# Optimization experiments

Measured on AMD Instinct MI355X. Metric: run time of the kernel, lower is better.

The kernel has to match this reference:

```python
import jax, jax.numpy as jnp
import numpy as np

L, E, S, H, D, V = 6, 384, 256, 6, 64, 65
FF = 4 * E


def _ln(x, g, b, ddof, eps=1e-5):
    mean = jnp.mean(x, axis=-1, keepdims=True)
    var = jnp.var(x, axis=-1, keepdims=True, ddof=ddof)
    return g * (x - mean) / jnp.sqrt(var + eps) + b


def setup_inputs() -> dict:
    key = jax.random.key(0)
    ks = jax.random.split(key, 16)
    std = 0.02
    inp = {
        'x': jax.random.randint(ks[0], (64, S), 0, V),
        'tok_emb': jax.random.normal(ks[1], (V, E)) * std,
        'pos_emb': jax.random.normal(ks[2], (S, E)) * std,
        'Wq': jax.random.normal(ks[3], (L, E, H * D)) * std,
        'Wk': jax.random.normal(ks[4], (L, E, H * D)) * std,
        'Wv': jax.random.normal(ks[5], (L, E, H * D)) * std,
        'Wproj': jax.random.normal(ks[6], (L, H * D, E)) * std,
        'bproj': jnp.zeros((L, E)),
        'W1': jax.random.normal(ks[7], (L, E, FF)) * std,
        'b1': jnp.zeros((L, FF)),
        'W2': jax.random.normal(ks[8], (L, FF, E)) * std,
        'b2': jnp.zeros((L, E)),
        'ln1_g': jnp.ones((L, E)), 'ln1_b': jnp.zeros((L, E)),
        'ln2_g': jnp.ones((L, E)), 'ln2_b': jnp.zeros((L, E)),
        'lnf_g': jnp.ones((E,)), 'lnf_b': jnp.zeros((E,)),
        'Wlm': jax.random.normal(ks[9], (E, V)) * std,
        'blm': jnp.zeros((V,)),
    }
    return inp


def _forward(x, tok_emb, pos_emb, Wq, Wk, Wv, Wproj, bproj, W1, b1, W2, b2,
             ln1_g, ln1_b, ln2_g, ln2_b, lnf_g, lnf_b, Wlm, blm):
    B, T = x.shape
    h = tok_emb[x] + pos_emb[:T]  # [B,T,E]
    causal = jnp.tril(jnp.ones((T, T), dtype=bool))
    neg_inf = jnp.finfo(h.dtype).min
    for l in range(L):
        hn = _ln(h, ln1_g[l], ln1_b[l], ddof=1)  # custom LayerNorm uses unbiased var
        q = (hn @ Wq[l]).reshape(B, T, H, D)
        k = (hn @ Wk[l]).reshape(B, T, H, D)
        v = (hn @ Wv[l]).reshape(B, T, H, D)
        wei = jnp.einsum('bqhd,bkhd->bhqk', q, k) * (D ** -0.5)
        wei = jnp.where(causal, wei, neg_inf)
        wei = jax.nn.softmax(wei, axis=-1)
        att = jnp.einsum('bhqk,bkhd->bqhd', wei, v).reshape(B, T, H * D)
        h = h + att @ Wproj[l] + bproj[l]
        hn = _ln(h, ln2_g[l], ln2_b[l], ddof=1)
        h = h + jax.nn.relu(hn @ W1[l] + b1[l]) @ W2[l] + b2[l]
    h = _ln(h, lnf_g, lnf_b, ddof=0)  # nn.LayerNorm uses biased var
    return h @ Wlm + blm  # logits [B,T,V]


def reference(x, tok_emb, pos_emb, Wq, Wk, Wv, Wproj, bproj, W1, b1, W2, b2,
              ln1_g, ln1_b, ln2_g, ln2_b, lnf_g, lnf_b, Wlm, blm):
    return _forward(x, tok_emb, pos_emb, Wq, Wk, Wv, Wproj, bproj, W1, b1, W2, b2,
                    ln1_g, ln1_b, ln2_g, ln2_b, lnf_g, lnf_b, Wlm, blm)
```

## Files before the change

### kernel.cpp

```cpp
#include <hip/hip_runtime.h>

#define L_  6
#define E_  384
#define T_  256
#define H_  6
#define D_  64
#define V_  65
#define FF_ 1536
#define B_  64
#define BT_ (B_*T_)
#define HD_ 384

typedef __attribute__((ext_vector_type(8))) short short8;
typedef __attribute__((ext_vector_type(4))) float f32x4;
typedef unsigned short us;
typedef unsigned int u32;

__device__ __forceinline__ us f2bf(float f) {
  u32 u = __float_as_uint(f);
  u32 r = (u + 0x7fffu + ((u >> 16) & 1u)) >> 16;
  return (us)r;
}
__device__ __forceinline__ float bf2f(us v) {
  return __uint_as_float(((u32)v) << 16);
}

__device__ __forceinline__ int xcd_swz(int b, int nwg) {
  const int q = nwg >> 3;
  return (b & 7) * q + (b >> 3);
}

__global__ void embed_kernel(const int* __restrict__ x, const float* __restrict__ tok,
                             const float* __restrict__ pos, us* __restrict__ h) {
  const int total8 = BT_ * E_ / 8;
  for (int i = blockIdx.x * blockDim.x + threadIdx.x; i < total8;
       i += gridDim.x * blockDim.x) {
    const int flat = i << 3;
    const int row  = flat / E_;
    const int e    = flat - row * E_;
    const int id   = x[row];
    const float4 a0 = *reinterpret_cast<const float4*>(tok + id * E_ + e);
    const float4 a1 = *reinterpret_cast<const float4*>(tok + id * E_ + e + 4);
    const float4 p0 = *reinterpret_cast<const float4*>(pos + (row & (T_ - 1)) * E_ + e);
    const float4 p1 = *reinterpret_cast<const float4*>(pos + (row & (T_ - 1)) * E_ + e + 4);
    short8 o;
    o[0] = (short)f2bf(a0.x + p0.x); o[1] = (short)f2bf(a0.y + p0.y);
    o[2] = (short)f2bf(a0.z + p0.z); o[3] = (short)f2bf(a0.w + p0.w);
    o[4] = (short)f2bf(a1.x + p1.x); o[5] = (short)f2bf(a1.y + p1.y);
    o[6] = (short)f2bf(a1.z + p1.z); o[7] = (short)f2bf(a1.w + p1.w);
    *reinterpret_cast<short8*>(h + flat) = o;
  }
}

template<int DDOF>
__global__ void stats_kernel(const us* __restrict__ h, float2* __restrict__ st) {
  const int wave = threadIdx.x >> 6;
  const int lane = threadIdx.x & 63;
  const int row  = (blockIdx.x << 2) + wave;
  float sum = 0.f, sq = 0.f;
  if (lane < 48) {
    const short8 v = *reinterpret_cast<const short8*>(h + (size_t)row * E_ + lane * 8);
#pragma unroll
    for (int j = 0; j < 8; ++j) {
      const float f = bf2f((us)v[j]);
      sum += f; sq += f * f;
    }
  }
#pragma unroll
  for (int off = 32; off > 0; off >>= 1) {
    sum += __shfl_xor(sum, off);
    sq  += __shfl_xor(sq, off);
  }
  if (lane == 0) {
    const float mean = sum * (1.f / E_);
    const float var  = (sq - E_ * mean * mean) * (1.f / (E_ - DDOF));
    float2 o; o.x = mean; o.y = rsqrtf(var + 1e-5f);
    st[row] = o;
  }
}

__global__ void transpose_w(const float* __restrict__ src, us* __restrict__ dst,
                            int K, int N, int Ndst, long srcLS, long dstLS,
                            const float* __restrict__ g) {
  __shared__ float t[32][33];
  const int n0 = blockIdx.x << 5, k0 = blockIdx.y << 5;
  const int tx = threadIdx.x & 31, ty = threadIdx.x >> 5;
  const float* s = src + (size_t)blockIdx.z * srcLS;
  us* d = dst + (size_t)blockIdx.z * dstLS;
#pragma unroll
  for (int j = 0; j < 32; j += 8) {
    const int n = n0 + tx;
    t[ty + j][tx] = (n < N) ? s[(size_t)(k0 + ty + j) * N + n] : 0.f;
  }
  __syncthreads();
  const float gk = g ? g[blockIdx.z * 384 + k0 + tx] : 1.f;
#pragma unroll
  for (int j = 0; j < 32; j += 8) {
    const int n = n0 + ty + j;
    if (n < Ndst) d[(size_t)n * K + k0 + tx] = f2bf(t[tx][ty + j] * gk);
  }
}

__global__ void transpose_qkv(const float* __restrict__ Wq, const float* __restrict__ Wk,
                              const float* __restrict__ Wv, us* __restrict__ dst,
                              const float* __restrict__ g) {
  __shared__ float t[32][33];
  const int sel = blockIdx.z / 6, l = blockIdx.z % 6;
  const float* s = (sel == 0 ? Wq : sel == 1 ? Wk : Wv) + (size_t)l * 147456;
  us* d = dst + (size_t)l * 442368 + sel * 147456;
  const int n0 = blockIdx.x << 5, k0 = blockIdx.y << 5;
  const int tx = threadIdx.x & 31, ty = threadIdx.x >> 5;
#pragma unroll
  for (int j = 0; j < 32; j += 8)
    t[ty + j][tx] = s[(size_t)(k0 + ty + j) * 384 + n0 + tx];
  __syncthreads();
  const float gk = g[l * 384 + k0 + tx];
#pragma unroll
  for (int j = 0; j < 32; j += 8)
    d[(size_t)(n0 + ty + j) * 384 + k0 + tx] = f2bf(t[tx][ty + j] * gk);
}

__global__ void c12_kernel(const float* __restrict__ W, const float* __restrict__ g,
                           const float* __restrict__ b, float2* __restrict__ out,
                           int N, long srcLS, int outLS) {
  __shared__ float p1[4][64], p2[4][64];
  const int t = threadIdx.x;
  const int c = t & 63, kq = t >> 6;
  const int n = (blockIdx.x << 6) + c;
  const float* Wz = W + (size_t)blockIdx.y * srcLS;
  const float* gz = g + blockIdx.y * 384;
  const float* bz = b + blockIdx.y * 384;
  float s1 = 0.f, s2 = 0.f;
  if (n < N) {
    for (int k = kq * 96; k < kq * 96 + 96; ++k) {
      const float w = Wz[(size_t)k * N + n];
      s1 = fmaf(gz[k], w, s1);
      s2 = fmaf(bz[k], w, s2);
    }
  }
  p1[kq][c] = s1; p2[kq][c] = s2;
  __syncthreads();
  if (t < 64) {
    const int nn = (blockIdx.x << 6) + t;
    if (nn < N) {
      float2 o;
      o.x = p1[0][t] + p1[1][t] + p1[2][t] + p1[3][t];
      o.y = p2[0][t] + p2[1][t] + p2[2][t] + p2[3][t];
      out[(size_t)blockIdx.y * outLS + nn] = o;
    }
  }
}

__global__ void c12_qkv(const float* __restrict__ Wq, const float* __restrict__ Wk,
                        const float* __restrict__ Wv, const float* __restrict__ g,
                        const float* __restrict__ b, float2* __restrict__ out) {
  __shared__ float p1[4][64], p2[4][64];
  const int sel = blockIdx.y / 6, l = blockIdx.y % 6;
  const float* Wz = (sel == 0 ? Wq : sel == 1 ? Wk : Wv) + (size_t)l * 147456;
  const float* gz = g + l * 384;
  const float* bz = b + l * 384;
  const int t = threadIdx.x;
  const int c = t & 63, kq = t >> 6;
  const int n = (blockIdx.x << 6) + c;
  float s1 = 0.f, s2 = 0.f;
  for (int k = kq * 96; k < kq * 96 + 96; ++k) {
    const float w = Wz[(size_t)k * 384 + n];
    s1 = fmaf(gz[k], w, s1);
    s2 = fmaf(bz[k], w, s2);
  }
  p1[kq][c] = s1; p2[kq][c] = s2;
  __syncthreads();
  if (t < 64) {
    const int nn = (blockIdx.x << 6) + t;
    float2 o;
    o.x = p1[0][t] + p1[1][t] + p1[2][t] + p1[3][t];
    o.y = p2[0][t] + p2[1][t] + p2[2][t] + p2[3][t];
    out[(size_t)l * 1152 + sel * 384 + nn] = o;
  }
}

template<int ROWS, int CHPR, int NTH>
__device__ __forceinline__ void stageG(const us* g, int rowUs, us* lds, int tid) {
#pragma unroll
  for (int j = 0; j < ROWS * CHPR / NTH; ++j) {
    const int fl  = j * NTH + tid;
    const int row = fl / CHPR;
    const int c   = fl % CHPR;
    const int gc  = (CHPR == 8) ? (c ^ (row & 7)) : (c ^ ((row >> 1) & 3));
    const us* src = g + (size_t)row * rowUs + gc * 8;
    __builtin_amdgcn_global_load_lds(
        (const __attribute__((address_space(1))) u32*)src,
        (__attribute__((address_space(3))) u32*)(lds + ((fl >> 6) << 9)),
        16, 0, 0);
  }
}

#define GEMM_LOOP(K_, NT_)                                                        \
  const int NT = (NT_);                                                           \
  _Pragma("unroll")                                                               \
  for (int p = 0; p < BUFS - 1; ++p) {                                            \
    stageG<BM, 4, 256>(Abase + p * 32, (K_), As[p], tid);                         \
    stageG<BN, 4, 256>(Bbase + p * 32, (K_), Bs[p], tid);                         \
  }                                                                               \
  int cb = 0;                                                                     \
  for (int t = 0; t < NT; ++t) {                                                  \
    if constexpr (BUFS == 4) {                                                    \
      if (t < NT - 2)       asm volatile("s_waitcnt vmcnt(%0)" :: "n"(2 * LPS) : "memory"); \
      else if (t == NT - 2) asm volatile("s_waitcnt vmcnt(%0)" :: "n"(LPS) : "memory");     \
      else                  asm volatile("s_waitcnt vmcnt(0)" ::: "memory");      \
    } else {                                                                      \
      if (t < NT - 1)       asm volatile("s_waitcnt vmcnt(%0)" :: "n"(LPS) : "memory");     \
      else                  asm volatile("s_waitcnt vmcnt(0)" ::: "memory");      \
    }                                                                             \
    __builtin_amdgcn_s_barrier();                                                 \
    __builtin_amdgcn_sched_barrier(0);                                            \
    if (t + BUFS - 1 < NT) {                                                      \
      int ib = cb + (BUFS - 1); if (ib >= BUFS) ib -= BUFS;                       \
      stageG<BM, 4, 256>(Abase + (t + BUFS - 1) * 32, (K_), As[ib], tid);         \
      stageG<BN, 4, 256>(Bbase + (t + BUFS - 1) * 32, (K_), Bs[ib], tid);         \
    }                                                                             \
    short8 af[FM], bfr[FN];                                                       \
    _Pragma("unroll")                                                             \
    for (int mt = 0; mt < FM; ++mt) {                                             \
      const int row = wm + mt * 16 + fm;                                          \
      af[mt] = *(const short8*)(As[cb] + row * 32 + ((fg ^ ((row >> 1) & 3)) << 3)); \
    }                                                                             \
    _Pragma("unroll")                                                             \
    for (int nt = 0; nt < FN; ++nt) {                                             \
      const int row = wn + nt * 16 + fm;                                          \
      bfr[nt] = *(const short8*)(Bs[cb] + row * 32 + ((fg ^ ((row >> 1) & 3)) << 3)); \
    }                                                                             \
    _Pragma("unroll")                                                             \
    for (int mt = 0; mt < FM; ++mt)                                               \
      _Pragma("unroll")                                                           \
      for (int nt = 0; nt < FN; ++nt)                                             \
        acc[mt][nt] = __builtin_amdgcn_mfma_f32_16x16x32_bf16(af[mt], bfr[nt], acc[mt][nt], 0, 0, 0); \
    cb = (cb + 1 == BUFS) ? 0 : cb + 1;                                           \
  }

template<int FM, int FN, int BUFS>
__global__ __launch_bounds__(256)
void gemm_mfma(const us* __restrict__ A, const us* __restrict__ Bt,
               const float* __restrict__ bias, const us* Res,
               us* __restrict__ O, int N, int K, int gx) {
  constexpr int BM = FM * 32, BN = FN * 32;
  constexpr int LPS = (BM + BN) * 4 / 256;
  __shared__ us As[BUFS][BM * 32];
  __shared__ us Bs[BUFS][BN * 32];
  const int tid = threadIdx.x;
  const int lid = xcd_swz(blockIdx.x, gridDim.x);
  const int bnI = lid % gx, bmI = lid / gx;
  const int bm = bmI * BM, bn = bnI * BN;
  const int wv = tid >> 6, ln = tid & 63;
  const int fm = ln & 15, fg = ln >> 4;
  const int wm = (wv >> 1) * (FM * 16), wn = (wv & 1) * (FN * 16);
  const us* Abase = A + (size_t)bm * K;
  const us* Bbase = Bt + (size_t)bn * K;

  f32x4 acc[FM][FN];
  const f32x4 zz = {0.f, 0.f, 0.f, 0.f};
#pragma unroll
  for (int i = 0; i < FM; ++i)
#pragma unroll
    for (int j = 0; j < FN; ++j) acc[i][j] = zz;

  GEMM_LOOP(K, K >> 5)

#pragma unroll
  for (int mt = 0; mt < FM; ++mt) {
#pragma unroll
    for (int nt = 0; nt < FN; ++nt) {
      const int col  = bn + wn + nt * 16 + fm;
      const int row0 = bm + wm + mt * 16 + fg * 4;
      const float bc = bias[col];
#pragma unroll
      for (int r = 0; r < 4; ++r) {
        const size_t idx = (size_t)(row0 + r) * N + col;
        O[idx] = f2bf(acc[mt][nt][r] + bc + bf2f(Res[idx]));
      }
    }
  }
}

template<int FM, int FN, int EPI, int BUFS>
__global__ __launch_bounds__(256)
void gemm_fold(const us* __restrict__ A, const us* __restrict__ Bt,
               const float2* __restrict__ st, const float2* __restrict__ c12,
               const float* __restrict__ bias, void* O0, void* O1,
               int N, int gx) {
  constexpr int K = 384;
  constexpr int BM = FM * 32, BN = FN * 32;
  constexpr int LPS = (BM + BN) * 4 / 256;
  __shared__ us As[BUFS][BM * 32];
  __shared__ us Bs[BUFS][BN * 32];
  const int tid = threadIdx.x;
  const int lid = xcd_swz(blockIdx.x, gridDim.x);
  const int bnI = lid % gx, bmI = lid / gx;
  const int bm = bmI * BM, bn = bnI * BN;
  const int wv = tid >> 6, ln = tid & 63;
  const int fm = ln & 15, fg = ln >> 4;
  const int wm = (wv >> 1) * (FM * 16), wn = (wv & 1) * (FN * 16);
  const us* Abase = A + (size_t)bm * K;
  const us* Bbase = Bt + (size_t)bn * K;

  f32x4 acc[FM][FN];
  const f32x4 zz = {0.f, 0.f, 0.f, 0.f};
#pragma unroll
  for (int i = 0; i < FM; ++i)
#pragma unroll
    for (int j = 0; j < FN; ++j) acc[i][j] = zz;

  GEMM_LOOP(K, 12)

#pragma unroll
  for (int mt = 0; mt < FM; ++mt) {
    const int row0 = bm + wm + mt * 16 + fg * 4;
    float2 sr[4];
#pragma unroll
    for (int r = 0; r < 4; ++r) sr[r] = st[row0 + r];
#pragma unroll
    for (int nt = 0; nt < FN; ++nt) {
      const int col = bn + wn + nt * 16 + fm;
      if (EPI == 3 && col >= V_) continue;
      const float2 cc = c12[col];
      float vals[4];
#pragma unroll
      for (int r = 0; r < 4; ++r)
        vals[r] = sr[r].y * (acc[mt][nt][r] - sr[r].x * cc.x) + cc.y;
      if (EPI == 0) {
        if (col < 768) {
          us* qk = (us*)O0;
#pragma unroll
          for (int r = 0; r < 4; ++r)
            qk[(size_t)(row0 + r) * 768 + col] = f2bf(vals[r]);
        } else {
          const int d = col - 768;
          const int hh = d >> 6, dd = d & 63;
          const int bI = row0 >> 8, t0 = row0 & 255;
          us* vt = (us*)O1;
          ushort4 pk;
          pk.x = f2bf(vals[0]); pk.y = f2bf(vals[1]);
          pk.z = f2bf(vals[2]); pk.w = f2bf(vals[3]);
          *reinterpret_cast<ushort4*>(vt + ((size_t)((bI * H_ + hh) * 64 + dd)) * 256 + t0) = pk;
        }
      } else if (EPI == 2) {
        us* o = (us*)O0;
        const float bc = bias[col];
#pragma unroll
        for (int r = 0; r < 4; ++r)
          o[(size_t)(row0 + r) * N + col] = f2bf(fmaxf(vals[r] + bc, 0.f));
      } else {
        float* o = (float*)O0;
        const float bc = bias[col];
#pragma unroll
        for (int r = 0; r < 4; ++r)
          o[(size_t)(row0 + r) * V_ + col] = vals[r] + bc;
      }
    }
  }
}

__global__ __launch_bounds__(256)
void attn_mfma(const us* __restrict__ qk, const us* __restrict__ vT,
               us* __restrict__ ab) {
  __shared__ us Ks[2][64 * 64];
  __shared__ us Vs[2][64 * 64];
  __shared__ us Plds[4][16 * 72];
  const int tid = threadIdx.x, w = tid >> 6, l = tid & 63;
  const int m = l & 15, g = l >> 4;
  const int bi = xcd_swz(blockIdx.x, gridDim.x);
  const int b = bi / 24, rem = bi - b * 24, h = rem >> 2, qt = rem & 3;
  const int qrow = (b << 8) + (qt << 6) + (w << 4);
  const us* Kg = qk + (size_t)(b << 8) * 768 + 384 + h * 64;
  const us* Vg = vT + (size_t)(b * H_ + h) * 64 * 256;

  short8 qf0, qf1;
  {
    const us* qp = qk + (size_t)(qrow + m) * 768 + h * 64 + g * 8;
    qf0 = *(const short8*)qp;
    qf1 = *(const short8*)(qp + 32);
  }
  float mrow[4], ssum[4];
  f32x4 o[4];
  const f32x4 zz = {0.f, 0.f, 0.f, 0.f};
#pragma unroll
  for (int r = 0; r < 4; ++r) { mrow[r] = -1e30f; ssum[r] = 0.f; o[r] = zz; }

  stageG<64, 8, 256>(Kg, 768, Ks[0], tid);
  stageG<64, 8, 256>(Vg, 256, Vs[0], tid);
  __syncthreads();

  int cur = 0;
  for (int kt = 0; kt <= qt; ++kt) {
    if (kt < qt) {
      stageG<64, 8, 256>(Kg + (size_t)(kt + 1) * 64 * 768, 768, Ks[cur ^ 1], tid);
      stageG<64, 8, 256>(Vg + (kt + 1) * 64,               256, Vs[cur ^ 1], tid);
    }
    f32x4 s[4];
#pragma unroll
    for (int nt = 0; nt < 4; ++nt) {
      const int row = nt * 16 + m;
      const int sw  = row & 7;
      short8 kf0 = *(const short8*)(Ks[cur] + row * 64 + ((g ^ sw) << 3));
      short8 kf1 = *(const short8*)(Ks[cur] + row * 64 + (((4 | g) ^ sw) << 3));
      f32x4 z = zz;
      z = __builtin_amdgcn_mfma_f32_16x16x32_bf16(qf0, kf0, z, 0, 0, 0);
      z = __builtin_amdgcn_mfma_f32_16x16x32_bf16(qf1, kf1, z, 0, 0, 0);
      s[nt] = z;
    }
    const bool diag = (kt == qt);
    float p[4][4], tmax[4];
#pragma unroll
    for (int r = 0; r < 4; ++r) tmax[r] = -1e30f;
#pragma unroll
    for (int nt = 0; nt < 4; ++nt)
#pragma unroll
      for (int r = 0; r < 4; ++r) {
        float v = s[nt][r] * 0.125f;
        if (diag) {
          const int key = nt * 16 + m;
          const int qq  = (w << 4) + (g << 2) + r;
          if (key > qq) v = -1e30f;
        }
        p[nt][r] = v;
        tmax[r] = fmaxf(tmax[r], v);
      }
#pragma unroll
    for (int xm = 1; xm < 16; xm <<= 1)
#pragma unroll
      for (int r = 0; r < 4; ++r) tmax[r] = fmaxf(tmax[r], __shfl_xor(tmax[r], xm));
    float sc[4], tsum[4];
#pragma unroll
    for (int r = 0; r < 4; ++r) {
      const float nm = fmaxf(mrow[r], tmax[r]);
      sc[r] = __expf(mrow[r] - nm);
      mrow[r] = nm;
      tsum[r] = 0.f;
    }
#pragma unroll
    for (int nt = 0; nt < 4; ++nt)
#pragma unroll
      for (int r = 0; r < 4; ++r) {
        p[nt][r] = __expf(p[nt][r] - mrow[r]);
        tsum[r] += p[nt][r];
      }
#pragma unroll
    for (int xm = 1; xm < 16; xm <<= 1)
#pragma unroll
      for (int r = 0; r < 4; ++r) tsum[r] += __shfl_xor(tsum[r], xm);
#pragma unroll
    for (int r = 0; r < 4; ++r) ssum[r] = ssum[r] * sc[r] + tsum[r];
#pragma unroll
    for (int nt = 0; nt < 4; ++nt)
#pragma unroll
      for (int r = 0; r < 4; ++r) o[nt][r] *= sc[r];
#pragma unroll
    for (int nt = 0; nt < 4; ++nt)
#pragma unroll
      for (int r = 0; r < 4; ++r)
        Plds[w][(g * 4 + r) * 72 + nt * 16 + m] = f2bf(p[nt][r]);
#pragma unroll
    for (int kc = 0; kc < 2; ++kc) {
      short8 pa = *(const short8*)&Plds[w][m * 72 + kc * 32 + g * 8];
#pragma unroll
      for (int nd = 0; nd < 4; ++nd) {
        const int row = nd * 16 + m;
        short8 vf = *(const short8*)(Vs[cur] + row * 64 + ((((kc << 2) | g) ^ (row & 7)) << 3));
        o[nd] = __builtin_amdgcn_mfma_f32_16x16x32_bf16(pa, vf, o[nd], 0, 0, 0);
      }
    }
    __syncthreads();
    cur ^= 1;
  }
#pragma unroll
  for (int r = 0; r < 4; ++r) {
    const float inv = 1.f / ssum[r];
    const size_t rowoff = (size_t)(qrow + g * 4 + r) * 384 + h * 64;
#pragma unroll
    for (int nd = 0; nd < 4; ++nd)
      ab[rowoff + nd * 16 + m] = f2bf(o[nd][r] * inv);
  }
}

extern "C" void kernel_launch(void* const* d_in, const int* in_sizes, int n_in,
                              void* d_out, int out_size, void* d_ws, size_t ws_size,
                              hipStream_t stream) {
  const int*   x    = (const int*)  d_in[0];
  const float* tok  = (const float*)d_in[1];
  const float* pos  = (const float*)d_in[2];
  const float* Wq   = (const float*)d_in[3];
  const float* Wk   = (const float*)d_in[4];
  const float* Wv   = (const float*)d_in[5];
  const float* Wpr  = (const float*)d_in[6];
  const float* bpr  = (const float*)d_in[7];
  const float* W1   = (const float*)d_in[8];
  const float* b1   = (const float*)d_in[9];
  const float* W2   = (const float*)d_in[10];
  const float* b2   = (const float*)d_in[11];
  const float* ln1g = (const float*)d_in[12];
  const float* ln1b = (const float*)d_in[13];
  const float* ln2g = (const float*)d_in[14];
  const float* ln2b = (const float*)d_in[15];
  const float* lnfg = (const float*)d_in[16];
  const float* lnfb = (const float*)d_in[17];
  const float* Wlm  = (const float*)d_in[18];
  const float* blm  = (const float*)d_in[19];
  float* out = (float*)d_out;

  char* W = (char*)d_ws;
  us*     h    = (us*)(W + 0);
  us*     qkb  = (us*)(W + 12582912);
  us*     vTb  = (us*)(W + 37748736);
  us*     abb  = (us*)(W + 50331648);
  us*     ffa  = (us*)(W + 12582912);
  us*     qkvT = (us*)(W + 62914560);
  us*     projT= (us*)(W + 68222976);
  us*     W1T  = (us*)(W + 69992448);
  us*     W2T  = (us*)(W + 77070336);
  us*     WlmT = (us*)(W + 84148224);
  float2* st   = (float2*)(W + 84246528);
  float2* c12q = (float2*)(W + 84377600);
  float2* c12f = (float2*)(W + 84432896);
  float2* c12lm= (float2*)(W + 84506624);

  transpose_qkv<<<dim3(12,12,18), 256, 0, stream>>>(Wq, Wk, Wv, qkvT, ln1g);
  transpose_w<<<dim3(12,12,6), 256, 0, stream>>>(Wpr, projT, 384, 384, 384, 147456, 147456, nullptr);
  transpose_w<<<dim3(48,12,6), 256, 0, stream>>>(W1,  W1T,   384, 1536, 1536, 589824, 589824, ln2g);
  transpose_w<<<dim3(12,48,6), 256, 0, stream>>>(W2,  W2T,   1536, 384, 384, 589824, 589824, nullptr);
  transpose_w<<<dim3(4,12,1),  256, 0, stream>>>(Wlm, WlmT,  384, 65, 128, 0, 0, lnfg);

  c12_qkv<<<dim3(6,18), 256, 0, stream>>>(Wq, Wk, Wv, ln1g, ln1b, c12q);
  c12_kernel<<<dim3(24,6), 256, 0, stream>>>(W1,  ln2g, ln2b, c12f,  1536, 589824, 1536);
  c12_kernel<<<dim3(2,1),  256, 0, stream>>>(Wlm, lnfg, lnfb, c12lm, 65, 0, 0);

  embed_kernel<<<3072, 256, 0, stream>>>(x, tok, pos, h);

  for (int l = 0; l < L_; ++l) {
    stats_kernel<1><<<BT_/4, 256, 0, stream>>>(h, st);
    gemm_fold<2,4,0,4><<<2304, 256, 0, stream>>>(
        h, qkvT + (size_t)l*442368, st, c12q + (size_t)l*1152, nullptr,
        qkb, vTb, 1152, 9);
    attn_mfma<<<B_*H_*4, 256, 0, stream>>>(qkb, vTb, abb);
    gemm_mfma<2,4,4><<<768, 256, 0, stream>>>(
        abb, projT + (size_t)l*147456, bpr + l*E_, h, h, 384, 384, 3);
    stats_kernel<1><<<BT_/4, 256, 0, stream>>>(h, st);
    gemm_fold<2,4,2,4><<<3072, 256, 0, stream>>>(
        h, W1T + (size_t)l*589824, st, c12f + (size_t)l*1536, b1 + l*FF_,
        ffa, nullptr, 1536, 12);
    gemm_mfma<2,4,4><<<768, 256, 0, stream>>>(
        ffa, W2T + (size_t)l*589824, b2 + l*E_, h, h, 384, 1536, 3);
  }

  stats_kernel<0><<<BT_/4, 256, 0, stream>>>(h, st);
  gemm_fold<2,4,3,4><<<256, 256, 0, stream>>>(
      h, WlmT, st, c12lm, blm, out, nullptr, 128, 1);
}
```

Before: 1.015 ms.

## Fuse LayerNorm row statistics into folded GEMM A-tile loads

Removes the separate stats kernels by accumulating per-row sum and sum of squares from the A fragments already loaded into registers during the GEMM main loop, then reducing across lanes with shuffles before the epilogue. This saves 13 kernel launches and an extra read pass over h per LayerNorm. The QKV and FF1 GEMMs also move to larger 128-row tiles with 3 buffers and half the grid, which changes occupancy and LDS usage. It adds ALU work inside the inner loop, and each block recomputes the row stats redundantly across N tiles.

```diff
diff --git a/kernel.cpp b/kernel.cpp
--- a/kernel.cpp
+++ b/kernel.cpp
@@ -52,33 +52,6 @@
   }
 }
 
-template<int DDOF>
-__global__ void stats_kernel(const us* __restrict__ h, float2* __restrict__ st) {
-  const int wave = threadIdx.x >> 6;
-  const int lane = threadIdx.x & 63;
-  const int row  = (blockIdx.x << 2) + wave;
-  float sum = 0.f, sq = 0.f;
-  if (lane < 48) {
-    const short8 v = *reinterpret_cast<const short8*>(h + (size_t)row * E_ + lane * 8);
-#pragma unroll
-    for (int j = 0; j < 8; ++j) {
-      const float f = bf2f((us)v[j]);
-      sum += f; sq += f * f;
-    }
-  }
-#pragma unroll
-  for (int off = 32; off > 0; off >>= 1) {
-    sum += __shfl_xor(sum, off);
-    sq  += __shfl_xor(sq, off);
-  }
-  if (lane == 0) {
-    const float mean = sum * (1.f / E_);
-    const float var  = (sq - E_ * mean * mean) * (1.f / (E_ - DDOF));
-    float2 o; o.x = mean; o.y = rsqrtf(var + 1e-5f);
-    st[row] = o;
-  }
-}
-
 __global__ void transpose_w(const float* __restrict__ src, us* __restrict__ dst,
                             int K, int N, int Ndst, long srcLS, long dstLS,
                             const float* __restrict__ g) {
@@ -195,7 +168,7 @@
   }
 }
 
-#define GEMM_LOOP(K_, NT_)                                                        \
+#define GEMM_LOOP(K_, NT_, STATS)                                                 \
   const int NT = (NT_);                                                           \
   _Pragma("unroll")                                                               \
   for (int p = 0; p < BUFS - 1; ++p) {                                            \
@@ -230,6 +203,16 @@
       const int row = wn + nt * 16 + fm;                                          \
       bfr[nt] = *(const short8*)(Bs[cb] + row * 32 + ((fg ^ ((row >> 1) & 3)) << 3)); \
     }                                                                             \
+    if (STATS) {                                                                  \
+      _Pragma("unroll")                                                           \
+      for (int mt = 0; mt < FM; ++mt)                                             \
+        _Pragma("unroll")                                                         \
+        for (int e = 0; e < 8; ++e) {                                             \
+          const float f_ = bf2f((us)af[mt][e]);                                   \
+          rsum[mt] += f_;                                                         \
+          rsq[mt]  = fmaf(f_, f_, rsq[mt]);                                       \
+        }                                                                         \
+    }                                                                             \
     _Pragma("unroll")                                                             \
     for (int mt = 0; mt < FM; ++mt)                                               \
       _Pragma("unroll")                                                           \
@@ -263,8 +246,11 @@
   for (int i = 0; i < FM; ++i)
 #pragma unroll
     for (int j = 0; j < FN; ++j) acc[i][j] = zz;
-
-  GEMM_LOOP(K, K >> 5)
+  float rsum[FM], rsq[FM];
+#pragma unroll
+  for (int i = 0; i < FM; ++i) { rsum[i] = 0.f; rsq[i] = 0.f; }
+
+  GEMM_LOOP(K, K >> 5, 0)
 
 #pragma unroll
   for (int mt = 0; mt < FM; ++mt) {
@@ -282,12 +268,11 @@
   }
 }
 
-template<int FM, int FN, int EPI, int BUFS>
+template<int FM, int FN, int EPI, int BUFS, int DDOF>
 __global__ __launch_bounds__(256)
 void gemm_fold(const us* __restrict__ A, const us* __restrict__ Bt,
-               const float2* __restrict__ st, const float2* __restrict__ c12,
-               const float* __restrict__ bias, void* O0, void* O1,
-               int N, int gx) {
+               const float2* __restrict__ c12, const float* __restrict__ bias,
+               void* O0, void* O1, int N, int gx) {
   constexpr int K = 384;
   constexpr int BM = FM * 32, BN = FN * 32;
   constexpr int LPS = (BM + BN) * 4 / 256;
@@ -309,15 +294,32 @@
   for (int i = 0; i < FM; ++i)
 #pragma unroll
     for (int j = 0; j < FN; ++j) acc[i][j] = zz;
-
-  GEMM_LOOP(K, 12)
+  float rsum[FM], rsq[FM];
+#pragma unroll
+  for (int i = 0; i < FM; ++i) { rsum[i] = 0.f; rsq[i] = 0.f; }
+
+  GEMM_LOOP(K, 12, 1)
+
+#pragma unroll
+  for (int mt = 0; mt < FM; ++mt) {
+    rsum[mt] += __shfl_xor(rsum[mt], 16);
+    rsum[mt] += __shfl_xor(rsum[mt], 32);
+    rsq[mt]  += __shfl_xor(rsq[mt], 16);
+    rsq[mt]  += __shfl_xor(rsq[mt], 32);
+  }
 
 #pragma unroll
   for (int mt = 0; mt < FM; ++mt) {
     const int row0 = bm + wm + mt * 16 + fg * 4;
-    float2 sr[4];
-#pragma unroll
-    for (int r = 0; r < 4; ++r) sr[r] = st[row0 + r];
+    float mu[4], iv[4];
+#pragma unroll
+    for (int r = 0; r < 4; ++r) {
+      const float s_ = __shfl(rsum[mt], (fg << 2) + r);
+      const float q_ = __shfl(rsq[mt],  (fg << 2) + r);
+      mu[r] = s_ * (1.f / 384.f);
+      const float var = (q_ - 384.f * mu[r] * mu[r]) * (1.f / (384 - DDOF));
+      iv[r] = rsqrtf(var + 1e-5f);
+    }
 #pragma unroll
     for (int nt = 0; nt < FN; ++nt) {
       const int col = bn + wn + nt * 16 + fm;
@@ -326,7 +328,7 @@
       float vals[4];
 #pragma unroll
       for (int r = 0; r < 4; ++r)
-        vals[r] = sr[r].y * (acc[mt][nt][r] - sr[r].x * cc.x) + cc.y;
+        vals[r] = iv[r] * (acc[mt][nt][r] - mu[r] * cc.x) + cc.y;
       if (EPI == 0) {
         if (col < 768) {
           us* qk = (us*)O0;
@@ -518,7 +520,6 @@
   us*     W1T  = (us*)(W + 69992448);
   us*     W2T  = (us*)(W + 77070336);
   us*     WlmT = (us*)(W + 84148224);
-  float2* st   = (float2*)(W + 84246528);
   float2* c12q = (float2*)(W + 84377600);
   float2* c12f = (float2*)(W + 84432896);
   float2* c12lm= (float2*)(W + 84506624);
@@ -536,22 +537,19 @@
   embed_kernel<<<3072, 256, 0, stream>>>(x, tok, pos, h);
 
   for (int l = 0; l < L_; ++l) {
-    stats_kernel<1><<<BT_/4, 256, 0, stream>>>(h, st);
-    gemm_fold<2,4,0,4><<<2304, 256, 0, stream>>>(
-        h, qkvT + (size_t)l*442368, st, c12q + (size_t)l*1152, nullptr,
+    gemm_fold<4,4,0,3,1><<<1152, 256, 0, stream>>>(
+        h, qkvT + (size_t)l*442368, c12q + (size_t)l*1152, nullptr,
         qkb, vTb, 1152, 9);
     attn_mfma<<<B_*H_*4, 256, 0, stream>>>(qkb, vTb, abb);
     gemm_mfma<2,4,4><<<768, 256, 0, stream>>>(
         abb, projT + (size_t)l*147456, bpr + l*E_, h, h, 384, 384, 3);
-    stats_kernel<1><<<BT_/4, 256, 0, stream>>>(h, st);
-    gemm_fold<2,4,2,4><<<3072, 256, 0, stream>>>(
-        h, W1T + (size_t)l*589824, st, c12f + (size_t)l*1536, b1 + l*FF_,
+    gemm_fold<4,4,2,3,1><<<1536, 256, 0, stream>>>(
+        h, W1T + (size_t)l*589824, c12f + (size_t)l*1536, b1 + l*FF_,
         ffa, nullptr, 1536, 12);
     gemm_mfma<2,4,4><<<768, 256, 0, stream>>>(
         ffa, W2T + (size_t)l*589824, b2 + l*E_, h, h, 384, 1536, 3);
   }
 
-  stats_kernel<0><<<BT_/4, 256, 0, stream>>>(h, st);
-  gemm_fold<2,4,3,4><<<256, 256, 0, stream>>>(
-      h, WlmT, st, c12lm, blm, out, nullptr, 128, 1);
-}
+  gemm_fold<2,4,3,4,0><<<256, 256, 0, stream>>>(
+      h, WlmT, c12lm, blm, out, nullptr, 128, 1);
+}
```

Measured after the change: 1.061 ms. +4.6%, slower.
